# Kernel tuning notes

Hardware: AMD Instinct MI355X
Metric: run time of the kernel (lower is better)

Reference implementation:

```python
import jax, jax.numpy as jnp
import numpy as np

B, S, E, H, U = 2048, 64, 512, 512, 512

def setup_inputs() -> dict:
    key = jax.random.key(0)
    ks = jax.random.split(key, 6)
    s = lambda d: 1.0 / np.sqrt(d)
    return {
        "features": jax.random.normal(ks[0], (B, S, E), jnp.float32),
        "hidden": jax.random.normal(ks[1], (B, H), jnp.float32),
        "W1": jax.random.normal(ks[2], (E, U), jnp.float32) * s(E),
        "b1": jnp.zeros((U,), jnp.float32),
        "W2": jax.random.normal(ks[3], (H, U), jnp.float32) * s(H),
        "b2": jnp.zeros((U,), jnp.float32),
        "Wv": jax.random.normal(ks[4], (U, 1), jnp.float32) * s(U),
        "bv": jnp.zeros((1,), jnp.float32),
    }

def reference(features, hidden, W1, b1, W2, b2, Wv, bv):
    # Bahdanau additive attention (dropout at inference = identity).
    h1 = jnp.einsum('bse,eu->bsu', features, W1) + b1          # [B,S,U]
    h2 = hidden @ W2 + b2                                       # [B,U]
    scores = jnp.tanh(h1 + h2[:, None, :]) @ Wv + bv            # [B,S,1]
    weights = jax.nn.softmax(scores, axis=1)                    # softmax over seq
    context = jnp.sum(weights * features, axis=1)               # [B,E]
    return context
```

## Files before the change

### kernel.cpp

```cpp
#include <hip/hip_runtime.h>

typedef _Float16 f16x8 __attribute__((ext_vector_type(8)));
typedef unsigned short u16x4 __attribute__((ext_vector_type(4)));
typedef float f32x4 __attribute__((ext_vector_type(4)));

#define VMWAIT(N) asm volatile("s_waitcnt vmcnt(" #N ")" ::: "memory")
#define LGKM0()   asm volatile("s_waitcnt lgkmcnt(0)" ::: "memory")
#define FENCE()   asm volatile("" ::: "memory")
#define RBAR()    do { FENCE(); __builtin_amdgcn_s_barrier(); FENCE(); } while (0)

__device__ __forceinline__ u16x4 cvt4(float4 v) {
    u16x4 h;
    h[0] = __builtin_bit_cast(unsigned short, (_Float16)v.x);
    h[1] = __builtin_bit_cast(unsigned short, (_Float16)v.y);
    h[2] = __builtin_bit_cast(unsigned short, (_Float16)v.z);
    h[3] = __builtin_bit_cast(unsigned short, (_Float16)v.w);
    return h;
}

__global__ void convert_w_kernel(const float* __restrict__ w1,
                                 const float* __restrict__ w2,
                                 unsigned short* __restrict__ w1img,
                                 unsigned short* __restrict__ w2img) {
    int u = blockIdx.x;
    int k = threadIdx.x + blockIdx.y * 256;
    size_t idx = (size_t)(k >> 5) * 16384 + (size_t)u * 32 + (k & 31);
    _Float16 h1 = (_Float16)w1[(size_t)k * 512 + u];
    _Float16 h2 = (_Float16)w2[(size_t)k * 512 + u];
    w1img[idx] = __builtin_bit_cast(unsigned short, h1);
    w2img[idx] = __builtin_bit_cast(unsigned short, h2);
}

__device__ __forceinline__ void stage_a64(const float* __restrict__ src,
                                          char* As, int tid) {
    const int row = tid >> 2, q = tid & 3;
    const float* p = src + (size_t)row * 512 + q * 4;
    const int sw2 = ((row >> 1) & 3) << 4;
    char* wb = As + row * 64;
    float4 va[4], vb[4];
#define AISS(V, G) { _Pragma("unroll") \
    for (int j_ = 0; j_ < 4; ++j_) V[j_] = *(const float4*)(p + ((G) * 4 + j_) * 16); }
#define APRC(V, G) { _Pragma("unroll") \
    for (int j_ = 0; j_ < 4; ++j_) { \
        const int i_ = (G) * 4 + j_; \
        *(u16x4*)(wb + (i_ >> 1) * 4096 + ((q * 8 + (i_ & 1) * 32) ^ sw2)) = cvt4(V[j_]); } }
    AISS(va, 0); AISS(vb, 1);
    VMWAIT(4); APRC(va, 0); AISS(va, 2);
    VMWAIT(4); APRC(vb, 1); AISS(vb, 3);
    VMWAIT(4); APRC(va, 2); AISS(va, 4);
    VMWAIT(4); APRC(vb, 3); AISS(vb, 5);
    VMWAIT(4); APRC(va, 4); AISS(va, 6);
    VMWAIT(4); APRC(vb, 5); AISS(vb, 7);
    VMWAIT(4); APRC(va, 6);
    VMWAIT(0); APRC(vb, 7);
#undef AISS
#undef APRC
}

__device__ __forceinline__ void chunk_gemm(const char* __restrict__ bcol,
                                           const char* As, const int* aoff,
                                           f32x4 acc[4][4]) {
    f16x8 brA[4], brB[4], afA[4], afB[4];
    #pragma unroll
    for (int i = 0; i < 4; ++i)
        #pragma unroll
        for (int j = 0; j < 4; ++j) acc[i][j] = (f32x4){0.f, 0.f, 0.f, 0.f};
    #pragma unroll
    for (int j = 0; j < 4; ++j) brA[j] = *(const f16x8*)(bcol + j * 1024);
    #pragma unroll
    for (int j = 0; j < 4; ++j) brB[j] = *(const f16x8*)(bcol + 32768 + j * 1024);
    #pragma unroll
    for (int i = 0; i < 4; ++i) afA[i] = *(const f16x8*)(As + aoff[i]);
    #pragma unroll
    for (int tt = 0; tt < 8; ++tt) {
        const int t0 = 2 * tt, t1 = t0 + 1;
        #pragma unroll
        for (int i = 0; i < 4; ++i)
            afB[i] = *(const f16x8*)(As + t1 * 4096 + aoff[i]);
        VMWAIT(4);
        #pragma unroll
        for (int i = 0; i < 4; ++i)
            #pragma unroll
            for (int j = 0; j < 4; ++j)
                acc[i][j] = __builtin_amdgcn_mfma_f32_16x16x32_f16(afA[i], brA[j], acc[i][j], 0, 0, 0);
        if (t0 < 14) {
            #pragma unroll
            for (int j = 0; j < 4; ++j)
                brA[j] = *(const f16x8*)(bcol + (t0 + 2) * 32768 + j * 1024);
        }
        if (t1 < 15) {
            #pragma unroll
            for (int i = 0; i < 4; ++i)
                afA[i] = *(const f16x8*)(As + (t1 + 1) * 4096 + aoff[i]);
        }
        if (t1 < 14) { VMWAIT(4); } else { VMWAIT(0); }
        #pragma unroll
        for (int i = 0; i < 4; ++i)
            #pragma unroll
            for (int j = 0; j < 4; ++j)
                acc[i][j] = __builtin_amdgcn_mfma_f32_16x16x32_f16(afB[i], brB[j], acc[i][j], 0, 0, 0);
        if (t1 < 14) {
            #pragma unroll
            for (int j = 0; j < 4; ++j)
                brB[j] = *(const f16x8*)(bcol + (t1 + 2) * 32768 + j * 1024);
        }
    }
}

__global__ __launch_bounds__(256, 2)
void h2_gemm_kernel(const float* __restrict__ hidden,
                    const char* __restrict__ w2img,
                    const float* __restrict__ b2,
                    float* __restrict__ h2o) {
    __shared__ char As[65536];
    const int tid = threadIdx.x, bm = blockIdx.x, bn = blockIdx.y;
    const int lane = tid & 63, wid = tid >> 6;
    const int lane16 = lane & 15, g = lane >> 4;
    stage_a64(hidden + (size_t)bm * 32768, As, tid);
    __syncthreads();
    int aoff[4];
    #pragma unroll
    for (int i = 0; i < 4; ++i)
        aoff[i] = (i * 16 + lane16) * 64 + ((g ^ ((lane16 >> 1) & 3)) << 4);
    const char* bcol = w2img + (size_t)(bn * 256 + wid * 64 + lane16) * 64 + g * 16;
    f32x4 acc[4][4];
    chunk_gemm(bcol, As, aoff, acc);
    #pragma unroll
    for (int j = 0; j < 4; ++j) {
        int col = bn * 256 + wid * 64 + j * 16 + lane16;
        float bb = b2[col];
        #pragma unroll
        for (int i = 0; i < 4; ++i)
            #pragma unroll
            for (int r = 0; r < 4; ++r)
                h2o[(size_t)(bm * 64 + i * 16 + g * 4 + r) * 512 + col] = acc[i][j][r] + bb;
    }
}

__device__ __forceinline__ void chunk64_lowreg(const char* __restrict__ bcol,
                                               const char* As, const int* aoff,
                                               f32x4 acc[4][4]) {
    f16x8 brE[4], brO[4];
    #pragma unroll
    for (int i = 0; i < 4; ++i)
        #pragma unroll
        for (int j = 0; j < 4; ++j) acc[i][j] = (f32x4){0.f, 0.f, 0.f, 0.f};
    #pragma unroll
    for (int j = 0; j < 4; ++j) brE[j] = *(const f16x8*)(bcol + j * 1024);
    #pragma unroll
    for (int j = 0; j < 4; ++j) brO[j] = *(const f16x8*)(bcol + 32768 + j * 1024);
    #pragma unroll
    for (int t = 0; t < 16; ++t) {
        f16x8 af[4];
        #pragma unroll
        for (int i = 0; i < 4; ++i)
            af[i] = *(const f16x8*)(As + t * 4096 + aoff[i]);
        if (t < 14) { VMWAIT(4); } else { VMWAIT(0); }
        LGKM0();
        if ((t & 1) == 0) {
            #pragma unroll
            for (int i = 0; i < 4; ++i)
                #pragma unroll
                for (int j = 0; j < 4; ++j)
                    acc[i][j] = __builtin_amdgcn_mfma_f32_16x16x32_f16(af[i], brE[j], acc[i][j], 0, 0, 0);
            FENCE();
            if (t < 14) {
                #pragma unroll
                for (int j = 0; j < 4; ++j)
                    brE[j] = *(const f16x8*)(bcol + (t + 2) * 32768 + j * 1024);
            }
        } else {
            #pragma unroll
            for (int i = 0; i < 4; ++i)
                #pragma unroll
                for (int j = 0; j < 4; ++j)
                    acc[i][j] = __builtin_amdgcn_mfma_f32_16x16x32_f16(af[i], brO[j], acc[i][j], 0, 0, 0);
            FENCE();
            if (t < 14) {
                #pragma unroll
                for (int j = 0; j < 4; ++j)
                    brO[j] = *(const f16x8*)(bcol + (t + 2) * 32768 + j * 1024);
            }
        }
        FENCE();
    }
}

__global__ __launch_bounds__(512, 4)
void fused_all_kernel(const float* __restrict__ feat,
                      const char* __restrict__ w1img,
                      const float* __restrict__ h2,
                      const float* __restrict__ b1,
                      const float* __restrict__ wv,
                      float* __restrict__ out) {
    __shared__ char As[65536];
    __shared__ float spl[64 * 8];
    __shared__ float wsm[64];
    __shared__ float cpart[512];

    const int tid = threadIdx.x, bm = blockIdx.x;
    const int lane16 = tid & 15, g = (tid >> 4) & 3;
    const int wid = tid >> 6;

    {
        const int row = tid >> 3, q = tid & 7;
        const float* p = feat + (size_t)bm * 32768 + (size_t)row * 512 + q * 4;
        char* wb = As + row * 64 + (((q >> 1) ^ ((row >> 1) & 3)) << 4) + (q & 1) * 8;
        float4 va[4], vb[4];
#define AISS(V, G) { _Pragma("unroll") \
    for (int j_ = 0; j_ < 4; ++j_) V[j_] = *(const float4*)(p + ((G) * 4 + j_) * 32); }
#define APRC(V, G) { _Pragma("unroll") \
    for (int j_ = 0; j_ < 4; ++j_) *(u16x4*)(wb + ((G) * 4 + j_) * 4096) = cvt4(V[j_]); }
        AISS(va, 0); AISS(vb, 1);
        VMWAIT(4); APRC(va, 0); AISS(va, 2);
        VMWAIT(4); APRC(vb, 1); AISS(vb, 3);
        VMWAIT(4); APRC(va, 2);
        VMWAIT(0); APRC(vb, 3);
#undef AISS
#undef APRC
    }
    LGKM0();
    RBAR();

    int aoff[4];
    #pragma unroll
    for (int i = 0; i < 4; ++i)
        aoff[i] = (i * 16 + lane16) * 64 + ((g ^ ((lane16 >> 1) & 3)) << 4);
    const char* bcol = w1img + (size_t)(wid * 64 + lane16) * 64 + g * 16;
    f32x4 acc[4][4];
    chunk64_lowreg(bcol, As, aoff, acc);

    float hhv[4], wvv[4];
    #pragma unroll
    for (int j = 0; j < 4; ++j) {
        int col = wid * 64 + j * 16 + lane16;
        hhv[j] = b1[col] + h2[(size_t)bm * 512 + col];
        wvv[j] = wv[col];
    }

    #pragma unroll
    for (int i = 0; i < 4; ++i)
        #pragma unroll
        for (int r = 0; r < 4; ++r) {
            float s = 0.f;
            #pragma unroll
            for (int j = 0; j < 4; ++j) {
                float h = acc[i][j][r] + hhv[j];
                float ex = __expf(2.f * h);
                s += (1.f - 2.f * __builtin_amdgcn_rcpf(ex + 1.f)) * wvv[j];
            }
            s += __shfl_xor(s, 1); s += __shfl_xor(s, 2);
            s += __shfl_xor(s, 4); s += __shfl_xor(s, 8);
            if (lane16 == 0) spl[(i * 16 + g * 4 + r) * 8 + wid] = s;
        }
    LGKM0();
    RBAR();

    if (tid < 64) {
        float s = ((spl[tid * 8 + 0] + spl[tid * 8 + 1]) + (spl[tid * 8 + 2] + spl[tid * 8 + 3])) +
                  ((spl[tid * 8 + 4] + spl[tid * 8 + 5]) + (spl[tid * 8 + 6] + spl[tid * 8 + 7]));
        float m = s;
        #pragma unroll
        for (int off = 32; off; off >>= 1) m = fmaxf(m, __shfl_xor(m, off));
        float e = __expf(s - m);
        float sum = e;
        #pragma unroll
        for (int off = 32; off; off >>= 1) sum += __shfl_xor(sum, off);
        wsm[tid] = e / sum;
        LGKM0();
    }
    RBAR();

    {
        const int t2 = tid & 255, half = tid >> 8;
        const int kst = t2 >> 4;
        const int base = kst * 4096 + (t2 & 3) * 4;
        const int ksl = (t2 >> 2) & 3;
        float ax = 0.f, ay = 0.f;
        #pragma unroll 8
        for (int si = 0; si < 32; ++si) {
            const int s = half * 32 + si;
            unsigned vv = *(const unsigned*)(As + base + s * 64 +
                                             ((ksl ^ ((s >> 1) & 3)) << 4));
            float w = wsm[s];
            ax += w * (float)__builtin_bit_cast(_Float16, (unsigned short)(vv & 0xffffu));
            ay += w * (float)__builtin_bit_cast(_Float16, (unsigned short)(vv >> 16));
        }
        if (half == 1) { cpart[t2 * 2] = ax; cpart[t2 * 2 + 1] = ay; }
        LGKM0();
        RBAR();
        if (half == 0) {
            ax += cpart[t2 * 2]; ay += cpart[t2 * 2 + 1];
            ((float2*)out)[(size_t)bm * 256 + t2] = make_float2(ax, ay);
        }
    }
}

extern "C" void kernel_launch(void* const* d_in, const int* in_sizes, int n_in,
                              void* d_out, int out_size, void* d_ws, size_t ws_size,
                              hipStream_t stream) {
    (void)in_sizes; (void)n_in; (void)out_size; (void)ws_size;
    const float* feat   = (const float*)d_in[0];
    const float* hidden = (const float*)d_in[1];
    const float* W1     = (const float*)d_in[2];
    const float* b1     = (const float*)d_in[3];
    const float* W2     = (const float*)d_in[4];
    const float* b2     = (const float*)d_in[5];
    const float* Wv     = (const float*)d_in[6];
    float* out = (float*)d_out;

    char* ws = (char*)d_ws;
    unsigned short* w1img = (unsigned short*)(ws);
    unsigned short* w2img = (unsigned short*)(ws + 524288);
    float* h2 = (float*)(ws + 1048576);

    convert_w_kernel<<<dim3(512, 2), dim3(256), 0, stream>>>(W1, W2, w1img, w2img);
    h2_gemm_kernel<<<dim3(32, 2), dim3(256), 0, stream>>>(hidden, (const char*)w2img, b2, h2);
    fused_all_kernel<<<dim3(2048), dim3(512), 0, stream>>>(feat, (const char*)w1img, h2, b1, Wv, out);
}
```

Baseline: 142.3 us.

## Replace manual waitcnt pipelining with compiler scheduling and stagger context reads

Removes the hand-written s_waitcnt/fence schedule in the feature staging and the MFMA loop, inlining the GEMM and letting the compiler place waits and barriers through __syncthreads. The feature load now issues all 16 float4 loads up front before converting them. The context reduction rotates each thread's starting sequence index to spread LDS bank accesses. The change trades explicit control of load/compute overlap for compiler scheduling, with possible extra register pressure from holding 16 float4 values.

```diff
diff --git a/kernel.cpp b/kernel.cpp
--- a/kernel.cpp
+++ b/kernel.cpp
@@ -6,8 +6,6 @@
 
 #define VMWAIT(N) asm volatile("s_waitcnt vmcnt(" #N ")" ::: "memory")
 #define LGKM0()   asm volatile("s_waitcnt lgkmcnt(0)" ::: "memory")
-#define FENCE()   asm volatile("" ::: "memory")
-#define RBAR()    do { FENCE(); __builtin_amdgcn_s_barrier(); FENCE(); } while (0)
 
 __device__ __forceinline__ u16x4 cvt4(float4 v) {
     u16x4 h;
@@ -137,55 +135,6 @@
     }
 }
 
-__device__ __forceinline__ void chunk64_lowreg(const char* __restrict__ bcol,
-                                               const char* As, const int* aoff,
-                                               f32x4 acc[4][4]) {
-    f16x8 brE[4], brO[4];
-    #pragma unroll
-    for (int i = 0; i < 4; ++i)
-        #pragma unroll
-        for (int j = 0; j < 4; ++j) acc[i][j] = (f32x4){0.f, 0.f, 0.f, 0.f};
-    #pragma unroll
-    for (int j = 0; j < 4; ++j) brE[j] = *(const f16x8*)(bcol + j * 1024);
-    #pragma unroll
-    for (int j = 0; j < 4; ++j) brO[j] = *(const f16x8*)(bcol + 32768 + j * 1024);
-    #pragma unroll
-    for (int t = 0; t < 16; ++t) {
-        f16x8 af[4];
-        #pragma unroll
-        for (int i = 0; i < 4; ++i)
-            af[i] = *(const f16x8*)(As + t * 4096 + aoff[i]);
-        if (t < 14) { VMWAIT(4); } else { VMWAIT(0); }
-        LGKM0();
-        if ((t & 1) == 0) {
-            #pragma unroll
-            for (int i = 0; i < 4; ++i)
-                #pragma unroll
-                for (int j = 0; j < 4; ++j)
-                    acc[i][j] = __builtin_amdgcn_mfma_f32_16x16x32_f16(af[i], brE[j], acc[i][j], 0, 0, 0);
-            FENCE();
-            if (t < 14) {
-                #pragma unroll
-                for (int j = 0; j < 4; ++j)
-                    brE[j] = *(const f16x8*)(bcol + (t + 2) * 32768 + j * 1024);
-            }
-        } else {
-            #pragma unroll
-            for (int i = 0; i < 4; ++i)
-                #pragma unroll
-                for (int j = 0; j < 4; ++j)
-                    acc[i][j] = __builtin_amdgcn_mfma_f32_16x16x32_f16(af[i], brO[j], acc[i][j], 0, 0, 0);
-            FENCE();
-            if (t < 14) {
-                #pragma unroll
-                for (int j = 0; j < 4; ++j)
-                    brO[j] = *(const f16x8*)(bcol + (t + 2) * 32768 + j * 1024);
-            }
-        }
-        FENCE();
-    }
-}
-
 __global__ __launch_bounds__(512, 4)
 void fused_all_kernel(const float* __restrict__ feat,
                       const char* __restrict__ w1img,
@@ -194,7 +143,7 @@
                       const float* __restrict__ wv,
                       float* __restrict__ out) {
     __shared__ char As[65536];
-    __shared__ float spl[64 * 8];
+    __shared__ float spl[512];
     __shared__ float wsm[64];
     __shared__ float cpart[512];
 
@@ -206,29 +155,61 @@
         const int row = tid >> 3, q = tid & 7;
         const float* p = feat + (size_t)bm * 32768 + (size_t)row * 512 + q * 4;
         char* wb = As + row * 64 + (((q >> 1) ^ ((row >> 1) & 3)) << 4) + (q & 1) * 8;
-        float4 va[4], vb[4];
-#define AISS(V, G) { _Pragma("unroll") \
-    for (int j_ = 0; j_ < 4; ++j_) V[j_] = *(const float4*)(p + ((G) * 4 + j_) * 32); }
-#define APRC(V, G) { _Pragma("unroll") \
-    for (int j_ = 0; j_ < 4; ++j_) *(u16x4*)(wb + ((G) * 4 + j_) * 4096) = cvt4(V[j_]); }
-        AISS(va, 0); AISS(vb, 1);
-        VMWAIT(4); APRC(va, 0); AISS(va, 2);
-        VMWAIT(4); APRC(vb, 1); AISS(vb, 3);
-        VMWAIT(4); APRC(va, 2);
-        VMWAIT(0); APRC(vb, 3);
-#undef AISS
-#undef APRC
-    }
-    LGKM0();
-    RBAR();
+        float4 v[16];
+        #pragma unroll
+        for (int j = 0; j < 16; ++j) v[j] = *(const float4*)(p + j * 32);
+        #pragma unroll
+        for (int j = 0; j < 16; ++j) *(u16x4*)(wb + j * 4096) = cvt4(v[j]);
+    }
+    __syncthreads();
 
     int aoff[4];
     #pragma unroll
     for (int i = 0; i < 4; ++i)
         aoff[i] = (i * 16 + lane16) * 64 + ((g ^ ((lane16 >> 1) & 3)) << 4);
     const char* bcol = w1img + (size_t)(wid * 64 + lane16) * 64 + g * 16;
+
     f32x4 acc[4][4];
-    chunk64_lowreg(bcol, As, aoff, acc);
+    #pragma unroll
+    for (int i = 0; i < 4; ++i)
+        #pragma unroll
+        for (int j = 0; j < 4; ++j) acc[i][j] = (f32x4){0.f, 0.f, 0.f, 0.f};
+    f16x8 brE[4], brO[4];
+    #pragma unroll
+    for (int j = 0; j < 4; ++j) brE[j] = *(const f16x8*)(bcol + j * 1024);
+    #pragma unroll
+    for (int j = 0; j < 4; ++j) brO[j] = *(const f16x8*)(bcol + 32768 + j * 1024);
+
+    #pragma unroll
+    for (int t = 0; t < 16; ++t) {
+        f16x8 af[4];
+        #pragma unroll
+        for (int i = 0; i < 4; ++i)
+            af[i] = *(const f16x8*)(As + t * 4096 + aoff[i]);
+        if ((t & 1) == 0) {
+            #pragma unroll
+            for (int i = 0; i < 4; ++i)
+                #pragma unroll
+                for (int j = 0; j < 4; ++j)
+                    acc[i][j] = __builtin_amdgcn_mfma_f32_16x16x32_f16(af[i], brE[j], acc[i][j], 0, 0, 0);
+            if (t < 14) {
+                #pragma unroll
+                for (int j = 0; j < 4; ++j)
+                    brE[j] = *(const f16x8*)(bcol + (t + 2) * 32768 + j * 1024);
+            }
+        } else {
+            #pragma unroll
+            for (int i = 0; i < 4; ++i)
+                #pragma unroll
+                for (int j = 0; j < 4; ++j)
+                    acc[i][j] = __builtin_amdgcn_mfma_f32_16x16x32_f16(af[i], brO[j], acc[i][j], 0, 0, 0);
+            if (t < 14) {
+                #pragma unroll
+                for (int j = 0; j < 4; ++j)
+                    brO[j] = *(const f16x8*)(bcol + (t + 2) * 32768 + j * 1024);
+            }
+        }
+    }
 
     float hhv[4], wvv[4];
     #pragma unroll
@@ -253,8 +234,7 @@
             s += __shfl_xor(s, 4); s += __shfl_xor(s, 8);
             if (lane16 == 0) spl[(i * 16 + g * 4 + r) * 8 + wid] = s;
         }
-    LGKM0();
-    RBAR();
+    __syncthreads();
 
     if (tid < 64) {
         float s = ((spl[tid * 8 + 0] + spl[tid * 8 + 1]) + (spl[tid * 8 + 2] + spl[tid * 8 + 3])) +
@@ -267,9 +247,8 @@
         #pragma unroll
         for (int off = 32; off; off >>= 1) sum += __shfl_xor(sum, off);
         wsm[tid] = e / sum;
-        LGKM0();
-    }
-    RBAR();
+    }
+    __syncthreads();
 
     {
         const int t2 = tid & 255, half = tid >> 8;
@@ -279,7 +258,7 @@
         float ax = 0.f, ay = 0.f;
         #pragma unroll 8
         for (int si = 0; si < 32; ++si) {
-            const int s = half * 32 + si;
+            const int s = half * 32 + ((si + kst) & 31);
             unsigned vv = *(const unsigned*)(As + base + s * 64 +
                                              ((ksl ^ ((s >> 1) & 3)) << 4));
             float w = wsm[s];
@@ -287,8 +266,7 @@
             ay += w * (float)__builtin_bit_cast(_Float16, (unsigned short)(vv >> 16));
         }
         if (half == 1) { cpart[t2 * 2] = ax; cpart[t2 * 2 + 1] = ay; }
-        LGKM0();
-        RBAR();
+        __syncthreads();
         if (half == 0) {
             ax += cpart[t2 * 2]; ay += cpart[t2 * 2 + 1];
             ((float2*)out)[(size_t)bm * 256 + t2] = make_float2(ax, ay);
```

New measurement: 148.7 us. 4.5% more time.

## Issue all feature loads up front and prefetch bias/h2/wv into LDS

Applied to the files above, without the earlier changes.

The A-tile staging now issues all 16 float4 feature loads at once instead of two rotating groups of four, so more memory requests are in flight, then converts in waitcnt-staged batches. The b1+h2 and wv epilogue operands are loaded at kernel start and staged in shared memory, which hides their global latency behind the feature loads rather than exposing it after the GEMM. The context-reduction loop also rotates the sequence index per k-stripe to spread LDS bank accesses. The cost is 64 live float4 registers during staging, which may pressure the 4-waves-per-SIMD launch bound, plus about 4 KB more LDS.

```diff
diff --git a/kernel.cpp b/kernel.cpp
--- a/kernel.cpp
+++ b/kernel.cpp
@@ -194,7 +194,9 @@
                       const float* __restrict__ wv,
                       float* __restrict__ out) {
     __shared__ char As[65536];
-    __shared__ float spl[64 * 8];
+    __shared__ float hhs[512];
+    __shared__ float wvs[512];
+    __shared__ float spl[512];
     __shared__ float wsm[64];
     __shared__ float cpart[512];
 
@@ -206,18 +208,29 @@
         const int row = tid >> 3, q = tid & 7;
         const float* p = feat + (size_t)bm * 32768 + (size_t)row * 512 + q * 4;
         char* wb = As + row * 64 + (((q >> 1) ^ ((row >> 1) & 3)) << 4) + (q & 1) * 8;
-        float4 va[4], vb[4];
-#define AISS(V, G) { _Pragma("unroll") \
-    for (int j_ = 0; j_ < 4; ++j_) V[j_] = *(const float4*)(p + ((G) * 4 + j_) * 32); }
-#define APRC(V, G) { _Pragma("unroll") \
-    for (int j_ = 0; j_ < 4; ++j_) *(u16x4*)(wb + ((G) * 4 + j_) * 4096) = cvt4(V[j_]); }
-        AISS(va, 0); AISS(vb, 1);
-        VMWAIT(4); APRC(va, 0); AISS(va, 2);
-        VMWAIT(4); APRC(vb, 1); AISS(vb, 3);
-        VMWAIT(4); APRC(va, 2);
-        VMWAIT(0); APRC(vb, 3);
-#undef AISS
-#undef APRC
+        float hb = b1[tid];
+        float hv = h2[(size_t)bm * 512 + tid];
+        float wv_ = wv[tid];
+        FENCE();
+        float4 v[16];
+        #pragma unroll
+        for (int j = 0; j < 16; ++j) v[j] = *(const float4*)(p + j * 32);
+        FENCE();
+        VMWAIT(16);
+        hhs[tid] = hb + hv;
+        wvs[tid] = wv_;
+        VMWAIT(12);
+        #pragma unroll
+        for (int j = 0; j < 4; ++j)  *(u16x4*)(wb + j * 4096) = cvt4(v[j]);
+        VMWAIT(8);
+        #pragma unroll
+        for (int j = 4; j < 8; ++j)  *(u16x4*)(wb + j * 4096) = cvt4(v[j]);
+        VMWAIT(4);
+        #pragma unroll
+        for (int j = 8; j < 12; ++j) *(u16x4*)(wb + j * 4096) = cvt4(v[j]);
+        VMWAIT(0);
+        #pragma unroll
+        for (int j = 12; j < 16; ++j) *(u16x4*)(wb + j * 4096) = cvt4(v[j]);
     }
     LGKM0();
     RBAR();
@@ -234,8 +247,8 @@
     #pragma unroll
     for (int j = 0; j < 4; ++j) {
         int col = wid * 64 + j * 16 + lane16;
-        hhv[j] = b1[col] + h2[(size_t)bm * 512 + col];
-        wvv[j] = wv[col];
+        hhv[j] = hhs[col];
+        wvv[j] = wvs[col];
     }
 
     #pragma unroll
@@ -279,7 +292,7 @@
         float ax = 0.f, ay = 0.f;
         #pragma unroll 8
         for (int si = 0; si < 32; ++si) {
-            const int s = half * 32 + si;
+            const int s = half * 32 + ((si + kst) & 31);
             unsigned vv = *(const unsigned*)(As + base + s * 64 +
                                              ((ksl ^ ((s >> 1) & 3)) << 4));
             float w = wsm[s];
```

Measured after the change: 141.3 us. Within noise of the previous version (-0.7%).
